# Performance work log

Measured on AMD Instinct MI355X. Metric: run time of the kernel, lower is better.

The kernel has to match this reference:

```python
import jax, jax.numpy as jnp
import numpy as np

B, C, H, W, N = 2, 64, 512, 512, 150000


def setup_inputs() -> dict:
    key = jax.random.key(0)
    k = jax.random.split(key, 6)
    return {
        "before_pseudoimages": jax.random.normal(k[0], (B, C, H, W), jnp.float32),
        "after_pseudoimages": jax.random.normal(k[1], (B, C, H, W), jnp.float32),
        "point_offsets": jax.random.normal(k[2], (B, N, 3), jnp.float32),
        "voxel_coords": jax.random.randint(k[3], (B, N, 3), 0, 512, jnp.int32),
        "W1": jax.random.normal(k[4], (131, 32), jnp.float32) * 0.08,
        "b1": jnp.zeros((32,), jnp.float32),
        "W2": jax.random.normal(k[5], (32, 3), jnp.float32) * 0.18,
        "b2": jnp.zeros((3,), jnp.float32),
    }


def reference(before_pseudoimages, after_pseudoimages, point_offsets, voxel_coords,
              W1, b1, W2, b2):
    # voxel_coords[..., 0] is the Z index, asserted == 0 in the original; unused.
    ys = voxel_coords[..., 1]  # [B, N]
    xs = voxel_coords[..., 2]  # [B, N]

    def gather(img, y, x):
        # img: [C, H, W] -> gathered [N, C]  (matches pseudoimage[:, y, x].T)
        return img[:, y, x].T

    before_vecs = jax.vmap(gather)(before_pseudoimages, ys, xs)  # [B, N, C]
    after_vecs = jax.vmap(gather)(after_pseudoimages, ys, xs)    # [B, N, C]
    feats = jnp.concatenate([before_vecs, after_vecs, point_offsets], axis=-1)  # [B, N, 131]

    h = jax.nn.gelu(jnp.einsum("bnf,fh->bnh", feats, W1) + b1, approximate=False)
    flow = jnp.einsum("bnh,ho->bno", h, W2) + b2  # [B, N, 3]
    return flow
```

## Files before the change

### kernel.cpp

```cpp
#include <hip/hip_runtime.h>
#include <math.h>

#define NCH   64
#define IMW   512
#define NPTS  150000
#define TOTAL (2 * NPTS)
#define IMHW  (512 * 512)
#define HID   32
#define NBINS 32768


__global__ __launch_bounds__(256) void hist_kernel(const int* __restrict__ coords,
                                                   int* __restrict__ hist) {
    int gid = blockIdx.x * blockDim.x + threadIdx.x;
    if (gid >= TOTAL) return;
    const int y = coords[gid * 3 + 1];
    const int x = coords[gid * 3 + 2];
    const int b = (gid >= NPTS) ? 1 : 0;
    const int key = (b << 14) | (y << 5) | (x >> 4);
    atomicAdd(&hist[key], 1);
}

__global__ __launch_bounds__(1024) void scan_kernel(const int* __restrict__ hist,
                                                    int* __restrict__ binPos) {
    __shared__ int lds[1024];
    const int t = threadIdx.x;
    const int base = t * 32;
    int loc[32];
    int s = 0;
    #pragma unroll
    for (int i = 0; i < 32; ++i) { loc[i] = s; s += hist[base + i]; }
    lds[t] = s;
    __syncthreads();
    for (int d = 1; d < 1024; d <<= 1) {
        int v = lds[t];
        int add = (t >= d) ? lds[t - d] : 0;
        __syncthreads();
        lds[t] = v + add;
        __syncthreads();
    }
    const int excl = lds[t] - s;
    #pragma unroll
    for (int i = 0; i < 32; ++i) binPos[base + i] = excl + loc[i];
}

__global__ __launch_bounds__(256) void scatter_kernel(const int* __restrict__ coords,
                                                      int* __restrict__ binPos,
                                                      int* __restrict__ perm) {
    int gid = blockIdx.x * blockDim.x + threadIdx.x;
    if (gid >= TOTAL) return;
    const int y = coords[gid * 3 + 1];
    const int x = coords[gid * 3 + 2];
    const int b = (gid >= NPTS) ? 1 : 0;
    const int key = (b << 14) | (y << 5) | (x >> 4);
    const int pos = atomicAdd(&binPos[key], 1);
    perm[pos] = gid;
}


__global__ __launch_bounds__(256) void ffd_kernel(
    const float* __restrict__ before,
    const float* __restrict__ after,
    const float* __restrict__ offsets,
    const int*   __restrict__ coords,
    const float* __restrict__ W1,
    const float* __restrict__ b1,
    const float* __restrict__ W2,
    const float* __restrict__ b2,
    const int*   __restrict__ perm,
    float*       __restrict__ out)
{
    int gid = blockIdx.x * blockDim.x + threadIdx.x;
    if (gid >= TOTAL) return;
    const int pid = perm ? perm[gid] : gid;

    const int b = (pid >= NPTS) ? 1 : 0;
    const long pbase = (long)pid * 3;

    const int y = coords[pbase + 1];
    const int x = coords[pbase + 2];

    float acc[HID];
    #pragma unroll
    for (int h = 0; h < HID; ++h) acc[h] = b1[h];

    const long img_off = (long)b * NCH * IMHW + (long)y * IMW + x;
    const float* bp = before + img_off;
    const float* ap = after  + img_off;

    float g[16];

    for (int cc = 0; cc < NCH; cc += 16) {
        #pragma unroll
        for (int j = 0; j < 16; ++j) g[j] = bp[(long)(cc + j) * IMHW];
        #pragma unroll
        for (int j = 0; j < 16; ++j) {
            const float* wrow = W1 + (cc + j) * HID;
            #pragma unroll
            for (int h = 0; h < HID; ++h) acc[h] = fmaf(g[j], wrow[h], acc[h]);
        }
    }
    for (int cc = 0; cc < NCH; cc += 16) {
        #pragma unroll
        for (int j = 0; j < 16; ++j) g[j] = ap[(long)(cc + j) * IMHW];
        #pragma unroll
        for (int j = 0; j < 16; ++j) {
            const float* wrow = W1 + (64 + cc + j) * HID;
            #pragma unroll
            for (int h = 0; h < HID; ++h) acc[h] = fmaf(g[j], wrow[h], acc[h]);
        }
    }
    #pragma unroll
    for (int k = 0; k < 3; ++k) {
        const float v = offsets[pbase + k];
        const float* wrow = W1 + (128 + k) * HID;
        #pragma unroll
        for (int h = 0; h < HID; ++h) acc[h] = fmaf(v, wrow[h], acc[h]);
    }

    #pragma unroll
    for (int h = 0; h < HID; ++h) {
        const float xh = acc[h];
        acc[h] = 0.5f * xh * (1.0f + erff(xh * 0.70710678118654752f));
    }

    float o0 = b2[0], o1 = b2[1], o2 = b2[2];
    #pragma unroll
    for (int h = 0; h < HID; ++h) {
        o0 = fmaf(acc[h], W2[h * 3 + 0], o0);
        o1 = fmaf(acc[h], W2[h * 3 + 1], o1);
        o2 = fmaf(acc[h], W2[h * 3 + 2], o2);
    }

    out[pbase + 0] = o0;
    out[pbase + 1] = o1;
    out[pbase + 2] = o2;
}

extern "C" void kernel_launch(void* const* d_in, const int* in_sizes, int n_in,
                              void* d_out, int out_size, void* d_ws, size_t ws_size,
                              hipStream_t stream) {
    const float* before  = (const float*)d_in[0];
    const float* after   = (const float*)d_in[1];
    const float* offsets = (const float*)d_in[2];
    const int*   coords  = (const int*)  d_in[3];
    const float* W1      = (const float*)d_in[4];
    const float* b1      = (const float*)d_in[5];
    const float* W2      = (const float*)d_in[6];
    const float* b2      = (const float*)d_in[7];
    float* out = (float*)d_out;

    const int block = 256;
    const int grid  = (TOTAL + block - 1) / block;

    const size_t need = (size_t)(2 * NBINS + TOTAL) * sizeof(int);

    if (ws_size >= need) {
        int* hist   = (int*)d_ws;
        int* binPos = hist + NBINS;
        int* perm   = binPos + NBINS;

        hipMemsetAsync(hist, 0, NBINS * sizeof(int), stream);
        hist_kernel<<<grid, block, 0, stream>>>(coords, hist);
        scan_kernel<<<1, 1024, 0, stream>>>(hist, binPos);
        scatter_kernel<<<grid, block, 0, stream>>>(coords, binPos, perm);
        ffd_kernel<<<grid, block, 0, stream>>>(before, after, offsets, coords,
                                               W1, b1, W2, b2, perm, out);
    } else {
        ffd_kernel<<<grid, block, 0, stream>>>(before, after, offsets, coords,
                                               W1, b1, W2, b2, nullptr, out);
    }
}
```

Before: 112.7 us.

## Split each point across two threads for before/after images with LDS reduction

Each point is now handled by two threads. One gathers and multiplies the before-image channels, the other the after-image channels, and the partial hidden sums are combined through shared memory before GELU and the output layer. The channel loads are double-buffered so that gathers for the next 16 channels are issued before the FMAs on the current ones. The aim is more memory-level parallelism for the scattered gathers and shorter per-thread serial chains, at the cost of twice the threads, a block-wide barrier, and LDS traffic.

```diff
diff --git a/kernel.cpp b/kernel.cpp
--- a/kernel.cpp
+++ b/kernel.cpp
@@ -58,6 +58,18 @@
 }
 
 
+#define LOADCH(buf, cbase)                                             \
+    _Pragma("unroll")                                                  \
+    for (int j = 0; j < 16; ++j) buf[j] = img_ptr[(long)((cbase) + j) * IMHW];
+
+#define FMACH(buf, cbase)                                              \
+    _Pragma("unroll")                                                  \
+    for (int j = 0; j < 16; ++j) {                                     \
+        const float* wr = w1b + ((cbase) + j) * HID;                   \
+        _Pragma("unroll")                                              \
+        for (int h = 0; h < HID; ++h) acc[h] = fmaf(buf[j], wr[h], acc[h]); \
+    }
+
 __global__ __launch_bounds__(256) void ffd_kernel(
     const float* __restrict__ before,
     const float* __restrict__ after,
@@ -70,71 +82,78 @@
     const int*   __restrict__ perm,
     float*       __restrict__ out)
 {
-    int gid = blockIdx.x * blockDim.x + threadIdx.x;
-    if (gid >= TOTAL) return;
-    const int pid = perm ? perm[gid] : gid;
+    __shared__ float xch[HID][128];
 
+    const int lp  = threadIdx.x & 127;
+    const int img = __builtin_amdgcn_readfirstlane(threadIdx.x >> 7);
+    const int gpt = blockIdx.x * 128 + lp;
+    const bool valid = gpt < TOTAL;
+
+    int pid = 0;
+    if (valid) pid = perm ? perm[gpt] : gpt;
+
+    const long pbase = (long)pid * 3;
+    int y = 0, x = 0;
+    if (valid) { y = coords[pbase + 1]; x = coords[pbase + 2]; }
     const int b = (pid >= NPTS) ? 1 : 0;
-    const long pbase = (long)pid * 3;
 
-    const int y = coords[pbase + 1];
-    const int x = coords[pbase + 2];
+    const float* img_ptr = (img ? after : before) +
+                           (long)b * NCH * IMHW + (long)y * IMW + x;
+    const float* w1b = W1 + img * 64 * HID;
 
     float acc[HID];
-    #pragma unroll
-    for (int h = 0; h < HID; ++h) acc[h] = b1[h];
-
-    const long img_off = (long)b * NCH * IMHW + (long)y * IMW + x;
-    const float* bp = before + img_off;
-    const float* ap = after  + img_off;
-
-    float g[16];
-
-    for (int cc = 0; cc < NCH; cc += 16) {
+    if (img == 0) {
+        float o0 = 0.f, o1 = 0.f, o2 = 0.f;
+        if (valid) { o0 = offsets[pbase]; o1 = offsets[pbase + 1]; o2 = offsets[pbase + 2]; }
+        const float* r0 = W1 + 128 * HID;
+        const float* r1 = W1 + 129 * HID;
+        const float* r2 = W1 + 130 * HID;
         #pragma unroll
-        for (int j = 0; j < 16; ++j) g[j] = bp[(long)(cc + j) * IMHW];
+        for (int h = 0; h < HID; ++h)
+            acc[h] = fmaf(o2, r2[h], fmaf(o1, r1[h], fmaf(o0, r0[h], b1[h])));
+    } else {
         #pragma unroll
-        for (int j = 0; j < 16; ++j) {
-            const float* wrow = W1 + (cc + j) * HID;
-            #pragma unroll
-            for (int h = 0; h < HID; ++h) acc[h] = fmaf(g[j], wrow[h], acc[h]);
-        }
-    }
-    for (int cc = 0; cc < NCH; cc += 16) {
-        #pragma unroll
-        for (int j = 0; j < 16; ++j) g[j] = ap[(long)(cc + j) * IMHW];
-        #pragma unroll
-        for (int j = 0; j < 16; ++j) {
-            const float* wrow = W1 + (64 + cc + j) * HID;
-            #pragma unroll
-            for (int h = 0; h < HID; ++h) acc[h] = fmaf(g[j], wrow[h], acc[h]);
-        }
-    }
-    #pragma unroll
-    for (int k = 0; k < 3; ++k) {
-        const float v = offsets[pbase + k];
-        const float* wrow = W1 + (128 + k) * HID;
-        #pragma unroll
-        for (int h = 0; h < HID; ++h) acc[h] = fmaf(v, wrow[h], acc[h]);
+        for (int h = 0; h < HID; ++h) acc[h] = 0.f;
     }
 
-    #pragma unroll
-    for (int h = 0; h < HID; ++h) {
-        const float xh = acc[h];
-        acc[h] = 0.5f * xh * (1.0f + erff(xh * 0.70710678118654752f));
+    if (valid) {
+        float g0[16], g1[16];
+        LOADCH(g0, 0)
+        LOADCH(g1, 16)
+        FMACH(g0, 0)
+        LOADCH(g0, 32)
+        FMACH(g1, 16)
+        LOADCH(g1, 48)
+        FMACH(g0, 32)
+        FMACH(g1, 48)
     }
 
-    float o0 = b2[0], o1 = b2[1], o2 = b2[2];
-    #pragma unroll
-    for (int h = 0; h < HID; ++h) {
-        o0 = fmaf(acc[h], W2[h * 3 + 0], o0);
-        o1 = fmaf(acc[h], W2[h * 3 + 1], o1);
-        o2 = fmaf(acc[h], W2[h * 3 + 2], o2);
+    if (img == 1) {
+        #pragma unroll
+        for (int h = 0; h < HID; ++h) xch[h][lp] = acc[h];
     }
+    __syncthreads();
+    if (img == 0 && valid) {
+        #pragma unroll
+        for (int h = 0; h < HID; ++h) acc[h] += xch[h][lp];
 
-    out[pbase + 0] = o0;
-    out[pbase + 1] = o1;
-    out[pbase + 2] = o2;
+        #pragma unroll
+        for (int h = 0; h < HID; ++h) {
+            const float xh = acc[h];
+            acc[h] = 0.5f * xh * (1.0f + erff(xh * 0.70710678118654752f));
+        }
+
+        float o0 = b2[0], o1 = b2[1], o2 = b2[2];
+        #pragma unroll
+        for (int h = 0; h < HID; ++h) {
+            o0 = fmaf(acc[h], W2[h * 3 + 0], o0);
+            o1 = fmaf(acc[h], W2[h * 3 + 1], o1);
+            o2 = fmaf(acc[h], W2[h * 3 + 2], o2);
+        }
+        out[pbase + 0] = o0;
+        out[pbase + 1] = o1;
+        out[pbase + 2] = o2;
+    }
 }
 
 extern "C" void kernel_launch(void* const* d_in, const int* in_sizes, int n_in,
@@ -151,7 +170,8 @@
     float* out = (float*)d_out;
 
     const int block = 256;
-    const int grid  = (TOTAL + block - 1) / block;
+    const int sgrid = (TOTAL + block - 1) / block;
+    const int fgrid = (TOTAL + 127) / 128;
 
     const size_t need = (size_t)(2 * NBINS + TOTAL) * sizeof(int);
 
@@ -161,13 +181,13 @@
         int* perm   = binPos + NBINS;
 
         hipMemsetAsync(hist, 0, NBINS * sizeof(int), stream);
-        hist_kernel<<<grid, block, 0, stream>>>(coords, hist);
+        hist_kernel<<<sgrid, block, 0, stream>>>(coords, hist);
         scan_kernel<<<1, 1024, 0, stream>>>(hist, binPos);
-        scatter_kernel<<<grid, block, 0, stream>>>(coords, binPos, perm);
-        ffd_kernel<<<grid, block, 0, stream>>>(before, after, offsets, coords,
-                                               W1, b1, W2, b2, perm, out);
+        scatter_kernel<<<sgrid, block, 0, stream>>>(coords, binPos, perm);
+        ffd_kernel<<<fgrid, block, 0, stream>>>(before, after, offsets, coords,
+                                                W1, b1, W2, b2, perm, out);
     } else {
-        ffd_kernel<<<grid, block, 0, stream>>>(before, after, offsets, coords,
-                                               W1, b1, W2, b2, nullptr, out);
+        ffd_kernel<<<fgrid, block, 0, stream>>>(before, after, offsets, coords,
+                                                W1, b1, W2, b2, nullptr, out);
     }
 }
```

After: 119.3 us. 5.9% more time.

## Compute first-layer activations densely per pixel cell, then finish MLP per point

Applied to the files above, without the earlier changes.

Replaces the per-point gather MLP with a cell kernel. Each block computes the first-layer image contribution for every pixel in 16 cells of 16 pixels, using fully coalesced channel reads, and stores the results in LDS. The block's sorted points then read their pixel's hidden vector from LDS, add the offset and bias terms, apply GELU and compute the output layer. This removes scattered gathers and repeated work for points that share a pixel, at the cost of computing the first layer for every pixel, including ones with no points.

```diff
diff --git a/kernel.cpp b/kernel.cpp
--- a/kernel.cpp
+++ b/kernel.cpp
@@ -8,6 +8,7 @@
 #define IMHW  (512 * 512)
 #define HID   32
 #define NBINS 32768
+#define CPB   16
 
 
 __global__ __launch_bounds__(256) void hist_kernel(const int* __restrict__ coords,
@@ -22,6 +23,7 @@
 }
 
 __global__ __launch_bounds__(1024) void scan_kernel(const int* __restrict__ hist,
+                                                    int* __restrict__ binStart,
                                                     int* __restrict__ binPos) {
     __shared__ int lds[1024];
     const int t = threadIdx.x;
@@ -41,7 +43,11 @@
     }
     const int excl = lds[t] - s;
     #pragma unroll
-    for (int i = 0; i < 32; ++i) binPos[base + i] = excl + loc[i];
+    for (int i = 0; i < 32; ++i) {
+        const int v = excl + loc[i];
+        binStart[base + i] = v;
+        binPos[base + i]   = v;
+    }
 }
 
 __global__ __launch_bounds__(256) void scatter_kernel(const int* __restrict__ coords,
@@ -58,7 +64,7 @@
 }
 
 
-__global__ __launch_bounds__(256) void ffd_kernel(
+__global__ __launch_bounds__(256) void ffd_cell_kernel(
     const float* __restrict__ before,
     const float* __restrict__ after,
     const float* __restrict__ offsets,
@@ -68,15 +74,111 @@
     const float* __restrict__ W2,
     const float* __restrict__ b2,
     const int*   __restrict__ perm,
+    const int*   __restrict__ binStart,
+    float*       __restrict__ out)
+{
+    __shared__ float himg[CPB * 16 * 33];
+
+    const int tid  = threadIdx.x;
+    const int cl   = tid >> 4;
+    const int xo   = tid & 15;
+    const int cell = blockIdx.x * CPB + cl;
+    const int b    = cell >> 14;
+    const int y    = (cell >> 5) & 511;
+    const int x    = (cell & 31) * 16 + xo;
+
+    const long pix = (long)b * (64L * IMHW) + (long)y * IMW + x;
+    const float* p0 = before + pix;
+    const float* p1 = after  + pix;
+
+    float acc[HID];
+    #pragma unroll
+    for (int h = 0; h < HID; ++h) acc[h] = 0.f;
+
+    float g[16];
+    #pragma unroll
+    for (int ck = 0; ck < 4; ++ck) {
+        #pragma unroll
+        for (int j = 0; j < 16; ++j) g[j] = p0[(long)(ck * 16 + j) * IMHW];
+        #pragma unroll
+        for (int j = 0; j < 16; ++j) {
+            const float* wr = W1 + (ck * 16 + j) * HID;
+            #pragma unroll
+            for (int h = 0; h < HID; ++h) acc[h] = fmaf(g[j], wr[h], acc[h]);
+        }
+    }
+    #pragma unroll
+    for (int ck = 0; ck < 4; ++ck) {
+        #pragma unroll
+        for (int j = 0; j < 16; ++j) g[j] = p1[(long)(ck * 16 + j) * IMHW];
+        #pragma unroll
+        for (int j = 0; j < 16; ++j) {
+            const float* wr = W1 + (64 + ck * 16 + j) * HID;
+            #pragma unroll
+            for (int h = 0; h < HID; ++h) acc[h] = fmaf(g[j], wr[h], acc[h]);
+        }
+    }
+
+    {
+        float* hp = &himg[(cl * 16 + xo) * 33];
+        #pragma unroll
+        for (int h = 0; h < HID; ++h) hp[h] = acc[h];
+    }
+    __syncthreads();
+
+    const int bfc   = blockIdx.x * CPB;
+    const int start = binStart[bfc];
+    const int end   = (bfc + CPB < NBINS) ? binStart[bfc + CPB] : TOTAL;
+
+    const float* r0 = W1 + 128 * HID;
+    const float* r1 = W1 + 129 * HID;
+    const float* r2 = W1 + 130 * HID;
+
+    for (int i = start + tid; i < end; i += 256) {
+        const int pid = perm[i];
+        const long pbase = (long)pid * 3;
+        const int py = coords[pbase + 1];
+        const int px = coords[pbase + 2];
+        const int pb = (pid >= NPTS) ? 1 : 0;
+        const int pcl = ((pb << 14) | (py << 5) | (px >> 4)) - bfc;
+        const float* hsrc = &himg[(pcl * 16 + (px & 15)) * 33];
+
+        const float o0 = offsets[pbase + 0];
+        const float o1 = offsets[pbase + 1];
+        const float o2 = offsets[pbase + 2];
+
+        float q0 = b2[0], q1 = b2[1], q2 = b2[2];
+        #pragma unroll
+        for (int h = 0; h < HID; ++h) {
+            float v = hsrc[h] + b1[h];
+            v = fmaf(o2, r2[h], fmaf(o1, r1[h], fmaf(o0, r0[h], v)));
+            v = 0.5f * v * (1.0f + erff(v * 0.70710678118654752f));
+            q0 = fmaf(v, W2[h * 3 + 0], q0);
+            q1 = fmaf(v, W2[h * 3 + 1], q1);
+            q2 = fmaf(v, W2[h * 3 + 2], q2);
+        }
+        out[pbase + 0] = q0;
+        out[pbase + 1] = q1;
+        out[pbase + 2] = q2;
+    }
+}
+
+
+__global__ __launch_bounds__(256) void ffd_naive_kernel(
+    const float* __restrict__ before,
+    const float* __restrict__ after,
+    const float* __restrict__ offsets,
+    const int*   __restrict__ coords,
+    const float* __restrict__ W1,
+    const float* __restrict__ b1,
+    const float* __restrict__ W2,
+    const float* __restrict__ b2,
     float*       __restrict__ out)
 {
     int gid = blockIdx.x * blockDim.x + threadIdx.x;
     if (gid >= TOTAL) return;
-    const int pid = perm ? perm[gid] : gid;
-
-    const int b = (pid >= NPTS) ? 1 : 0;
-    const long pbase = (long)pid * 3;
-
+    const int b = (gid >= NPTS) ? 1 : 0;
+    const long pbase = (long)gid * 3;
     const int y = coords[pbase + 1];
     const int x = coords[pbase + 2];
 
@@ -84,57 +186,41 @@
     #pragma unroll
     for (int h = 0; h < HID; ++h) acc[h] = b1[h];
 
-    const long img_off = (long)b * NCH * IMHW + (long)y * IMW + x;
+    const long img_off = (long)b * (64L * IMHW) + (long)y * IMW + x;
     const float* bp = before + img_off;
     const float* ap = after  + img_off;
 
-    float g[16];
-
-    for (int cc = 0; cc < NCH; cc += 16) {
-        #pragma unroll
-        for (int j = 0; j < 16; ++j) g[j] = bp[(long)(cc + j) * IMHW];
-        #pragma unroll
-        for (int j = 0; j < 16; ++j) {
-            const float* wrow = W1 + (cc + j) * HID;
-            #pragma unroll
-            for (int h = 0; h < HID; ++h) acc[h] = fmaf(g[j], wrow[h], acc[h]);
-        }
-    }
-    for (int cc = 0; cc < NCH; cc += 16) {
-        #pragma unroll
-        for (int j = 0; j < 16; ++j) g[j] = ap[(long)(cc + j) * IMHW];
-        #pragma unroll
-        for (int j = 0; j < 16; ++j) {
-            const float* wrow = W1 + (64 + cc + j) * HID;
-            #pragma unroll
-            for (int h = 0; h < HID; ++h) acc[h] = fmaf(g[j], wrow[h], acc[h]);
-        }
+    for (int c = 0; c < NCH; ++c) {
+        const float v = bp[(long)c * IMHW];
+        const float* wr = W1 + c * HID;
+        #pragma unroll
+        for (int h = 0; h < HID; ++h) acc[h] = fmaf(v, wr[h], acc[h]);
+    }
+    for (int c = 0; c < NCH; ++c) {
+        const float v = ap[(long)c * IMHW];
+        const float* wr = W1 + (64 + c) * HID;
+        #pragma unroll
+        for (int h = 0; h < HID; ++h) acc[h] = fmaf(v, wr[h], acc[h]);
     }
     #pragma unroll
     for (int k = 0; k < 3; ++k) {
         const float v = offsets[pbase + k];
-        const float* wrow = W1 + (128 + k) * HID;
-        #pragma unroll
-        for (int h = 0; h < HID; ++h) acc[h] = fmaf(v, wrow[h], acc[h]);
-    }
-
+        const float* wr = W1 + (128 + k) * HID;
+        #pragma unroll
+        for (int h = 0; h < HID; ++h) acc[h] = fmaf(v, wr[h], acc[h]);
+    }
+    float q0 = b2[0], q1 = b2[1], q2 = b2[2];
     #pragma unroll
     for (int h = 0; h < HID; ++h) {
         const float xh = acc[h];
-        acc[h] = 0.5f * xh * (1.0f + erff(xh * 0.70710678118654752f));
-    }
-
-    float o0 = b2[0], o1 = b2[1], o2 = b2[2];
-    #pragma unroll
-    for (int h = 0; h < HID; ++h) {
-        o0 = fmaf(acc[h], W2[h * 3 + 0], o0);
-        o1 = fmaf(acc[h], W2[h * 3 + 1], o1);
-        o2 = fmaf(acc[h], W2[h * 3 + 2], o2);
-    }
-
-    out[pbase + 0] = o0;
-    out[pbase + 1] = o1;
-    out[pbase + 2] = o2;
+        const float v = 0.5f * xh * (1.0f + erff(xh * 0.70710678118654752f));
+        q0 = fmaf(v, W2[h * 3 + 0], q0);
+        q1 = fmaf(v, W2[h * 3 + 1], q1);
+        q2 = fmaf(v, W2[h * 3 + 2], q2);
+    }
+    out[pbase + 0] = q0;
+    out[pbase + 1] = q1;
+    out[pbase + 2] = q2;
 }
 
 extern "C" void kernel_launch(void* const* d_in, const int* in_sizes, int n_in,
@@ -151,23 +237,24 @@
     float* out = (float*)d_out;
 
     const int block = 256;
-    const int grid  = (TOTAL + block - 1) / block;
-
-    const size_t need = (size_t)(2 * NBINS + TOTAL) * sizeof(int);
+    const int sgrid = (TOTAL + block - 1) / block;
+
+    const size_t need = (size_t)(3 * NBINS + TOTAL) * sizeof(int);
 
     if (ws_size >= need) {
-        int* hist   = (int*)d_ws;
-        int* binPos = hist + NBINS;
-        int* perm   = binPos + NBINS;
+        int* hist     = (int*)d_ws;
+        int* binStart = hist + NBINS;
+        int* binPos   = binStart + NBINS;
+        int* perm     = binPos + NBINS;
 
         hipMemsetAsync(hist, 0, NBINS * sizeof(int), stream);
-        hist_kernel<<<grid, block, 0, stream>>>(coords, hist);
-        scan_kernel<<<1, 1024, 0, stream>>>(hist, binPos);
-        scatter_kernel<<<grid, block, 0, stream>>>(coords, binPos, perm);
-        ffd_kernel<<<grid, block, 0, stream>>>(before, after, offsets, coords,
-                                               W1, b1, W2, b2, perm, out);
+        hist_kernel<<<sgrid, block, 0, stream>>>(coords, hist);
+        scan_kernel<<<1, 1024, 0, stream>>>(hist, binStart, binPos);
+        scatter_kernel<<<sgrid, block, 0, stream>>>(coords, binPos, perm);
+        ffd_cell_kernel<<<NBINS / CPB, block, 0, stream>>>(
+            before, after, offsets, coords, W1, b1, W2, b2, perm, binStart, out);
     } else {
-        ffd_kernel<<<grid, block, 0, stream>>>(before, after, offsets, coords,
-                                               W1, b1, W2, b2, nullptr, out);
-    }
-}
+        ffd_naive_kernel<<<sgrid, block, 0, stream>>>(before, after, offsets, coords,
+                                                      W1, b1, W2, b2, out);
+    }
+}
```

New measurement: 151.5 us. 34.5% more time.
